# Optimization experiments

Hardware: AMD Instinct MI355X
Metric: run time of the kernel (lower is better)

## Reference

```python
import jax, jax.numpy as jnp
import numpy as np

D_MODEL = 1024
N_HEADS = 16
D_HEAD = 64
SCALE = D_HEAD ** -0.5


def setup_inputs() -> dict:
    key = jax.random.key(0)
    k1, k2, k3 = jax.random.split(key, 3)
    B, N = 4, 2048
    x = jax.random.normal(k1, (B, N, D_MODEL), dtype=jnp.float32)
    # NOTE: original torch module overwrites to_q three times, so q/k/v share ONE projection.
    W_qkv = jax.random.normal(k2, (D_MODEL, N_HEADS * D_HEAD), dtype=jnp.float32) * (D_MODEL ** -0.5)
    W_out = jax.random.normal(k3, (N_HEADS * D_HEAD, D_MODEL), dtype=jnp.float32) * (D_MODEL ** -0.5)
    b_out = jnp.zeros((D_MODEL,), dtype=jnp.float32)
    return {"x": x, "W_qkv": W_qkv, "W_out": W_out, "b_out": b_out}


def reference(x, W_qkv, W_out, b_out):
    B, N, _ = x.shape
    # shared projection (faithful to the to_q bug): q = k = v
    qkv = x @ W_qkv                                   # [B, N, H*D]
    q = qkv.reshape(B, N, N_HEADS, D_HEAD).transpose(0, 2, 1, 3)  # [B, H, N, D]
    k = q
    v = q
    scores = jnp.einsum('bhid,bhjd->bhij', q, k) * SCALE          # [B, H, N, N]
    attn = jax.nn.softmax(scores, axis=-1)
    out = jnp.einsum('bhij,bhjd->bhid', attn, v)                  # [B, H, N, D]
    out = out.transpose(0, 2, 1, 3).reshape(B, N, N_HEADS * D_HEAD)
    return out @ W_out + b_out
```

## Files before the change

### kernel.cpp

```cpp
#include <hip/hip_runtime.h>

typedef float  f32x4  __attribute__((ext_vector_type(4)));
typedef __bf16 bf16x8 __attribute__((ext_vector_type(8)));
typedef __bf16 bf16x4 __attribute__((ext_vector_type(4)));
typedef unsigned short u16x8 __attribute__((ext_vector_type(8)));

__device__ __forceinline__ unsigned short f2bf(float f) {
    unsigned u = __builtin_bit_cast(unsigned, f);
    unsigned r = u + 0x7FFFu + ((u >> 16) & 1u);
    return (unsigned short)(r >> 16);
}

__device__ __forceinline__ f32x4 mfma16(bf16x8 a, bf16x8 b, f32x4 c) {
    return __builtin_amdgcn_mfma_f32_16x16x32_bf16(a, b, c, 0, 0, 0);
}
__device__ __forceinline__ f32x4 mfma16u(u16x8 a, u16x8 b, f32x4 c) {
    return __builtin_amdgcn_mfma_f32_16x16x32_bf16(
        __builtin_bit_cast(bf16x8, a), __builtin_bit_cast(bf16x8, b), c, 0, 0, 0);
}

__device__ __forceinline__ float fexp2(float x) {
    float r;
    asm("v_exp_f32 %0, %1" : "=v"(r) : "v"(x));
    return r;
}

__device__ __forceinline__ void gload16(const void* g, void* l) {
    __builtin_amdgcn_global_load_lds((const __attribute__((address_space(1))) void*)g,
                                     (__attribute__((address_space(3))) void*)l,
                                     16, 0, 0);
}

__global__ __launch_bounds__(256) void cast_transpose2(const float* __restrict__ W0,
                                                       const float* __restrict__ W1,
                                                       __bf16* __restrict__ T0Q,
                                                       __bf16* __restrict__ T1Q) {
    const float* W = blockIdx.z ? W1 : W0;
    __bf16* Wt = blockIdx.z ? T1Q : T0Q;
    __shared__ __bf16 T[64][64];
    const int tid = threadIdx.x;
    const int k0 = blockIdx.y * 64, n0 = blockIdx.x * 64;
#pragma unroll
    for (int c = 0; c < 4; ++c) {
        int idx = c * 256 + tid;
        int kr = idx >> 4, nc = (idx & 15) * 4;
        f32x4 w = *(const f32x4*)&W[(size_t)(k0 + kr) * 1024 + n0 + nc];
        int g = ((nc >> 3) ^ (kr >> 3)) * 8 + (nc & 7);
        bf16x4 pk;
        pk[0] = (__bf16)w[0]; pk[1] = (__bf16)w[1];
        pk[2] = (__bf16)w[2]; pk[3] = (__bf16)w[3];
        *(bf16x4*)&T[kr][g] = pk;
    }
    __syncthreads();
#pragma unroll
    for (int c = 0; c < 2; ++c) {
        int idx = c * 256 + tid;
        int n = idx >> 3, k8 = (idx & 7) * 8;
        bf16x8 o;
#pragma unroll
        for (int e = 0; e < 8; ++e) {
            int k = k8 + e;
            o[e] = T[k][((n >> 3) ^ (k >> 3)) * 8 + (n & 7)];
        }
        *(bf16x8*)&Wt[(size_t)(n0 + n) * 1024 + k0 + k8] = o;
    }
}

template <bool OUT_BF16, bool WRITE_VT, bool CAST_A>
__global__ __launch_bounds__(256) void gemm_bt(const void* __restrict__ Av,
                                               const unsigned short* __restrict__ Bt,
                                               void* __restrict__ Cout,
                                               const float* __restrict__ bias,
                                               __bf16* __restrict__ vT) {
    constexpr int K = 1024, NN = 1024;
    __shared__ unsigned short SM[18432];
    typedef unsigned short u16_72[72];
    u16_72* As = (u16_72*)SM;
    u16_72* Bs = (u16_72*)(SM + 9216);
    const int tid  = threadIdx.x;
    const int lane = tid & 63, wid = tid >> 6;
    const int wm = wid >> 1, wn = wid & 1;
    const int i = lane & 15, q8 = (lane >> 4) * 8;
    const int bid = blockIdx.y * 8 + blockIdx.x;
    const int swz = (bid & 7) * 64 + (bid >> 3);
    const int tm = (swz >> 3) * 128, tn = (swz & 7) * 128;
    const int srow = tid >> 3, scol = (tid & 7) * 8;

    f32x4 acc[4][4] = {};

    for (int k0 = 0; k0 < K; k0 += 64) {
#pragma unroll
        for (int c = 0; c < 4; ++c) {
            int row = c * 32 + srow;
            u16x8 av;
            if constexpr (CAST_A) {
                const float* Af = (const float*)Av;
                const float* p = &Af[(size_t)(tm + row) * K + k0 + scol];
                f32x4 a0 = *(const f32x4*)p;
                f32x4 a1 = *(const f32x4*)(p + 4);
                av[0] = f2bf(a0[0]); av[1] = f2bf(a0[1]);
                av[2] = f2bf(a0[2]); av[3] = f2bf(a0[3]);
                av[4] = f2bf(a1[0]); av[5] = f2bf(a1[1]);
                av[6] = f2bf(a1[2]); av[7] = f2bf(a1[3]);
            } else {
                const unsigned short* Au = (const unsigned short*)Av;
                av = *(const u16x8*)&Au[(size_t)(tm + row) * K + k0 + scol];
            }
            u16x8 bv = *(const u16x8*)&Bt[(size_t)(tn + row) * K + k0 + scol];
            *(u16x8*)&As[row][scol] = av;
            *(u16x8*)&Bs[row][scol] = bv;
        }
        __syncthreads();
#pragma unroll
        for (int ks = 0; ks < 2; ++ks) {
            u16x8 af[4], bfr[4];
#pragma unroll
            for (int m = 0; m < 4; ++m) af[m]  = *(const u16x8*)&As[wm * 64 + m * 16 + i][ks * 32 + q8];
#pragma unroll
            for (int nn = 0; nn < 4; ++nn) bfr[nn] = *(const u16x8*)&Bs[wn * 64 + nn * 16 + i][ks * 32 + q8];
#pragma unroll
            for (int m = 0; m < 4; ++m)
#pragma unroll
                for (int nn = 0; nn < 4; ++nn)
                    acc[m][nn] = mfma16u(af[m], bfr[nn], acc[m][nn]);
        }
        __syncthreads();
    }

    const int r0 = (lane >> 4) * 4;
#pragma unroll
    for (int nn = 0; nn < 4; ++nn) {
        int col = tn + wn * 64 + nn * 16 + i;
        float bv = 0.f;
        if constexpr (!OUT_BF16) bv = bias[col];
#pragma unroll
        for (int m = 0; m < 4; ++m) {
            int rowb = tm + wm * 64 + m * 16 + r0;
#pragma unroll
            for (int r = 0; r < 4; ++r) {
                if constexpr (OUT_BF16)
                    ((unsigned short*)Cout)[(size_t)(rowb + r) * NN + col] = f2bf(acc[m][nn][r]);
                else
                    ((float*)Cout)[(size_t)(rowb + r) * NN + col] = acc[m][nn][r] + bv;
            }
        }
    }

    if constexpr (WRITE_VT) {
        unsigned short* T = SM;
#pragma unroll
        for (int nn = 0; nn < 4; ++nn) {
            const int col = wn * 64 + nn * 16 + i;
            const int g = col >> 3, c7 = col & 7;
#pragma unroll
            for (int m = 0; m < 4; ++m) {
                const int rbase = wm * 64 + m * 16 + r0;
                const int rsw = (rbase >> 3) & 15;
#pragma unroll
                for (int r = 0; r < 4; ++r)
                    T[(rbase + r) * 128 + ((g ^ rsw) * 8) + c7] = f2bf(acc[m][nn][r]);
            }
        }
        __syncthreads();
        const size_t vb0 = ((size_t)(tm >> 11) * 16 + (tn >> 6)) * 131072 + (size_t)(tm & 2047);
#pragma unroll
        for (int c = 0; c < 8; ++c) {
            int idx = c * 256 + tid;
            int hh = idx >> 10, dd = (idx >> 4) & 63, n8 = (idx & 15) * 8;
            int g = (hh * 64 + dd) >> 3, c7 = dd & 7, rsw = idx & 15;
            u16x8 o;
#pragma unroll
            for (int e = 0; e < 8; ++e)
                o[e] = T[(n8 + e) * 128 + ((g ^ rsw) * 8) + c7];
            *(u16x8*)&vT[vb0 + (size_t)hh * 131072 + (size_t)dd * 2048 + n8] = o;
        }
    }
}

__global__ __launch_bounds__(256, 4) void flash_attn7(const __bf16* __restrict__ qkv,
                                                      const __bf16* __restrict__ vT,
                                                      __bf16* __restrict__ attnout) {
    __shared__ __bf16 Ks[2][4096];
    __shared__ __bf16 Vs[2][4096];

    const int tid = threadIdx.x, lane = tid & 63, wid = tid >> 6;
    const int i = lane & 15, qg = lane >> 4;

    const int n = blockIdx.x;
    const int j = n & 7, t = n >> 3;
    const int head = j * 8 + (t >> 4);
    const int b = head >> 4, h = head & 15;
    const int q0 = (t & 15) * 128;

    const size_t base  = (size_t)b * (2048 * 1024) + (size_t)h * 64;
    const size_t vbase = (size_t)head * (64 * 2048);

    bf16x8 qf[2][2];
#pragma unroll
    for (int g = 0; g < 2; ++g) {
        int qrow = q0 + wid * 32 + g * 16 + i;
#pragma unroll
        for (int s = 0; s < 2; ++s)
            qf[g][s] = *(const bf16x8*)&qkv[base + (size_t)qrow * 1024 + s * 32 + qg * 8];
    }

    const int r0s = tid >> 3, g0s = tid & 7;
    const __bf16* ksrc0 = &qkv[base + (size_t)r0s * 1024 + (size_t)((g0s ^ (r0s & 7)) * 8)];
    const __bf16* ksrc1 = ksrc0 + 32 * 1024;
    const __bf16* vsrc0 = &vT[vbase + (size_t)r0s * 2048 + (size_t)((g0s ^ (r0s & 7)) * 8)];
    const __bf16* vsrc1 = vsrc0 + 32 * 2048;

    auto STAGE = [&](int buf) {
        gload16(ksrc0, &Ks[buf][wid * 512]);
        gload16(ksrc1, &Ks[buf][2048 + wid * 512]);
        gload16(vsrc0, &Vs[buf][wid * 512]);
        gload16(vsrc1, &Vs[buf][2048 + wid * 512]);
        ksrc0 += 64 * 1024; ksrc1 += 64 * 1024;
        vsrc0 += 64;        vsrc1 += 64;
    };

    const float SL2E = 0.18033688f;
    f32x4 po[2][4] = {};
    f32x4 po5[2]   = {};
    bf16x8 ones;
#pragma unroll
    for (int e = 0; e < 8; ++e) ones[e] = (__bf16)1.0f;

    auto BODY = [&](const __bf16* Kb, const __bf16* Vb) {
        __builtin_amdgcn_s_setprio(1);
        f32x4 st[2][4];
#pragma unroll
        for (int m = 0; m < 4; ++m) {
            bf16x8 kf0 = *(const bf16x8*)&Kb[(m * 16 + i) * 64 + ((qg) ^ (i & 7)) * 8];
            bf16x8 kf1 = *(const bf16x8*)&Kb[(m * 16 + i) * 64 + ((4 + qg) ^ (i & 7)) * 8];
            f32x4 z0 = {}, z1 = {};
            z0 = mfma16(kf0, qf[0][0], z0);
            st[0][m] = mfma16(kf1, qf[0][1], z0);
            z1 = mfma16(kf0, qf[1][0], z1);
            st[1][m] = mfma16(kf1, qf[1][1], z1);
        }
        __builtin_amdgcn_s_setprio(0);

        bf16x8 pa[2][2];
#pragma unroll
        for (int g = 0; g < 2; ++g) {
#pragma unroll
            for (int m = 0; m < 4; ++m)
#pragma unroll
                for (int r = 0; r < 4; ++r)
                    st[g][m][r] = fexp2(st[g][m][r] * SL2E);

#pragma unroll
            for (int r = 0; r < 4; ++r) {
                pa[g][0][r]     = (__bf16)st[g][0][r];
                pa[g][0][4 + r] = (__bf16)st[g][1][r];
                pa[g][1][r]     = (__bf16)st[g][2][r];
                pa[g][1][4 + r] = (__bf16)st[g][3][r];
            }
        }

        __builtin_amdgcn_s_setprio(1);
#pragma unroll
        for (int s = 0; s < 2; ++s) {
#pragma unroll
            for (int nf = 0; nf < 4; ++nf) {
                const int row = nf * 16 + i;
                bf16x8 vf;
                *(bf16x4*)&vf = *(const bf16x4*)
                    &Vb[row * 64 + (((s * 4 + (qg >> 1)) ^ (i & 7)) * 8 + (qg & 1) * 4)];
                *((bf16x4*)&vf + 1) = *(const bf16x4*)
                    &Vb[row * 64 + (((s * 4 + 2 + (qg >> 1)) ^ (i & 7)) * 8 + (qg & 1) * 4)];
                po[0][nf] = mfma16(pa[0][s], vf, po[0][nf]);
                po[1][nf] = mfma16(pa[1][s], vf, po[1][nf]);
            }
            po5[0] = mfma16(pa[0][s], ones, po5[0]);
            po5[1] = mfma16(pa[1][s], ones, po5[1]);
        }
        __builtin_amdgcn_s_setprio(0);
    };

    STAGE(0);
    __syncthreads();
    for (int kt2 = 0; kt2 < 16; ++kt2) {
        STAGE(1);
        BODY(Ks[0], Vs[0]);
        __syncthreads();
        if (kt2 < 15) STAGE(0);
        BODY(Ks[1], Vs[1]);
        __syncthreads();
    }

#pragma unroll
    for (int g = 0; g < 2; ++g) {
        float linv[4];
#pragma unroll
        for (int r = 0; r < 4; ++r) linv[r] = __builtin_amdgcn_rcpf(po5[g][r]);
#pragma unroll
        for (int nf = 0; nf < 4; ++nf)
#pragma unroll
            for (int r = 0; r < 4; ++r) {
                int row = q0 + wid * 32 + g * 16 + qg * 4 + r;
                attnout[base + (size_t)row * 1024 + nf * 16 + i] = (__bf16)(po[g][nf][r] * linv[r]);
            }
    }
}

extern "C" void kernel_launch(void* const* d_in, const int* in_sizes, int n_in,
                              void* d_out, int out_size, void* d_ws, size_t ws_size,
                              hipStream_t stream) {
    const float* x    = (const float*)d_in[0];
    const float* Wqkv = (const float*)d_in[1];
    const float* Wout = (const float*)d_in[2];
    const float* bout = (const float*)d_in[3];
    float* out = (float*)d_out;

    char* ws = (char*)d_ws;
    unsigned short* aout = (unsigned short*)(ws);
    unsigned short* qkvb = (unsigned short*)(ws + (16u << 20));
    __bf16*         vTp  = (__bf16*)(ws + (32u << 20));
    __bf16*         wqt  = (__bf16*)(ws + (48u << 20));
    __bf16*         wot  = (__bf16*)(ws + (50u << 20));

    cast_transpose2<<<dim3(16, 16, 2), 256, 0, stream>>>(Wqkv, Wout, wqt, wot);

    gemm_bt<true, true, true><<<dim3(8, 64), 256, 0, stream>>>(x, (const unsigned short*)wqt,
                                                               qkvb, nullptr, vTp);

    flash_attn7<<<1024, 256, 0, stream>>>((const __bf16*)qkvb, vTp, (__bf16*)aout);

    gemm_bt<false, false, false><<<dim3(8, 64), 256, 0, stream>>>(aout, (const unsigned short*)wot,
                                                                  out, bout, nullptr);
}
```

Before: 141.9 us.

## Use direct global-to-LDS loads with XOR swizzle in GEMM; prescale Q

The GEMM kernel now stages tiles through direct global-to-LDS buffer loads into an XOR-swizzled unpadded layout. Register round-trips and the padding are gone, though the cast path still converts A through registers. The attention kernel folds the softmax scale into Q when loading it, which removes a multiply per score element. The risk is a slight precision change from rounding the scaled Q to bf16.

New measurement: 140.7 us. No clear change (-0.9%).

```diff
diff --git a/kernel.cpp b/kernel.cpp
--- a/kernel.cpp
+++ b/kernel.cpp
@@ -73,61 +73,75 @@
                                                const float* __restrict__ bias,
                                                __bf16* __restrict__ vT) {
     constexpr int K = 1024, NN = 1024;
-    __shared__ unsigned short SM[18432];
-    typedef unsigned short u16_72[72];
-    u16_72* As = (u16_72*)SM;
-    u16_72* Bs = (u16_72*)(SM + 9216);
+    __shared__ unsigned short SM[16384];
     const int tid  = threadIdx.x;
     const int lane = tid & 63, wid = tid >> 6;
     const int wm = wid >> 1, wn = wid & 1;
-    const int i = lane & 15, q8 = (lane >> 4) * 8;
+    const int i = lane & 15, qg = lane >> 4;
     const int bid = blockIdx.y * 8 + blockIdx.x;
     const int swz = (bid & 7) * 64 + (bid >> 3);
     const int tm = (swz >> 3) * 128, tn = (swz & 7) * 128;
+
+    const int rl  = wid * 32 + (lane >> 3);
+    const int gsw = ((lane & 7) ^ (rl & 7)) * 8;
+    const unsigned short* Bsrc = &Bt[(size_t)(tn + rl) * K + gsw];
+    const unsigned short* Asrc = &((const unsigned short*)Av)[(size_t)(tm + rl) * K + gsw];
     const int srow = tid >> 3, scol = (tid & 7) * 8;
+    const float* Afsrc = &((const float*)Av)[(size_t)(tm + srow) * K + scol];
+    const int acol = ((scol >> 3) ^ (srow & 7)) * 8;
 
     f32x4 acc[4][4] = {};
 
-    for (int k0 = 0; k0 < K; k0 += 64) {
+    auto STAGE = [&]() {
 #pragma unroll
         for (int c = 0; c < 4; ++c) {
-            int row = c * 32 + srow;
-            u16x8 av;
             if constexpr (CAST_A) {
-                const float* Af = (const float*)Av;
-                const float* p = &Af[(size_t)(tm + row) * K + k0 + scol];
+                int row = c * 32 + srow;
+                const float* p = Afsrc + (size_t)c * 32 * K;
                 f32x4 a0 = *(const f32x4*)p;
                 f32x4 a1 = *(const f32x4*)(p + 4);
+                u16x8 av;
                 av[0] = f2bf(a0[0]); av[1] = f2bf(a0[1]);
                 av[2] = f2bf(a0[2]); av[3] = f2bf(a0[3]);
                 av[4] = f2bf(a1[0]); av[5] = f2bf(a1[1]);
                 av[6] = f2bf(a1[2]); av[7] = f2bf(a1[3]);
+                *(u16x8*)&SM[row * 64 + acol] = av;
             } else {
-                const unsigned short* Au = (const unsigned short*)Av;
-                av = *(const u16x8*)&Au[(size_t)(tm + row) * K + k0 + scol];
-            }
-            u16x8 bv = *(const u16x8*)&Bt[(size_t)(tn + row) * K + k0 + scol];
-            *(u16x8*)&As[row][scol] = av;
-            *(u16x8*)&Bs[row][scol] = bv;
-        }
-        __syncthreads();
+                gload16(Asrc + (size_t)c * 8 * K, &SM[(wid * 32 + c * 8) * 64]);
+            }
+            gload16(Bsrc + (size_t)c * 8 * K, &SM[8192 + (wid * 32 + c * 8) * 64]);
+        }
+        Afsrc += 64; Asrc += 64; Bsrc += 64;
+    };
+
+    auto COMP = [&]() {
+        const unsigned short* As = SM;
+        const unsigned short* Bs = SM + 8192;
 #pragma unroll
         for (int ks = 0; ks < 2; ++ks) {
             u16x8 af[4], bfr[4];
 #pragma unroll
-            for (int m = 0; m < 4; ++m) af[m]  = *(const u16x8*)&As[wm * 64 + m * 16 + i][ks * 32 + q8];
-#pragma unroll
-            for (int nn = 0; nn < 4; ++nn) bfr[nn] = *(const u16x8*)&Bs[wn * 64 + nn * 16 + i][ks * 32 + q8];
+            for (int m = 0; m < 4; ++m)
+                af[m]  = *(const u16x8*)&As[(wm * 64 + m * 16 + i) * 64 + (((ks * 4 + qg) ^ (i & 7)) * 8)];
+#pragma unroll
+            for (int nn = 0; nn < 4; ++nn)
+                bfr[nn] = *(const u16x8*)&Bs[(wn * 64 + nn * 16 + i) * 64 + (((ks * 4 + qg) ^ (i & 7)) * 8)];
 #pragma unroll
             for (int m = 0; m < 4; ++m)
 #pragma unroll
                 for (int nn = 0; nn < 4; ++nn)
                     acc[m][nn] = mfma16u(af[m], bfr[nn], acc[m][nn]);
         }
-        __syncthreads();
-    }
-
-    const int r0 = (lane >> 4) * 4;
+    };
+
+    for (int kk = 0; kk < 16; ++kk) {
+        STAGE();
+        __syncthreads();
+        COMP();
+        __syncthreads();
+    }
+
+    const int r0 = qg * 4;
 #pragma unroll
     for (int nn = 0; nn < 4; ++nn) {
         int col = tn + wn * 64 + nn * 16 + i;
@@ -177,7 +191,7 @@
     }
 }
 
-__global__ __launch_bounds__(256, 4) void flash_attn7(const __bf16* __restrict__ qkv,
+__global__ __launch_bounds__(256, 4) void flash_attn9(const __bf16* __restrict__ qkv,
                                                       const __bf16* __restrict__ vT,
                                                       __bf16* __restrict__ attnout) {
     __shared__ __bf16 Ks[2][4096];
@@ -195,13 +209,19 @@
     const size_t base  = (size_t)b * (2048 * 1024) + (size_t)h * 64;
     const size_t vbase = (size_t)head * (64 * 2048);
 
+    const float SL2E = 0.18033688f;
+
     bf16x8 qf[2][2];
 #pragma unroll
     for (int g = 0; g < 2; ++g) {
         int qrow = q0 + wid * 32 + g * 16 + i;
 #pragma unroll
-        for (int s = 0; s < 2; ++s)
-            qf[g][s] = *(const bf16x8*)&qkv[base + (size_t)qrow * 1024 + s * 32 + qg * 8];
+        for (int s = 0; s < 2; ++s) {
+            bf16x8 tq = *(const bf16x8*)&qkv[base + (size_t)qrow * 1024 + s * 32 + qg * 8];
+#pragma unroll
+            for (int e = 0; e < 8; ++e)
+                qf[g][s][e] = (__bf16)((float)tq[e] * SL2E);
+        }
     }
 
     const int r0s = tid >> 3, g0s = tid & 7;
@@ -219,7 +239,6 @@
         vsrc0 += 64;        vsrc1 += 64;
     };
 
-    const float SL2E = 0.18033688f;
     f32x4 po[2][4] = {};
     f32x4 po5[2]   = {};
     bf16x8 ones;
@@ -248,7 +267,7 @@
             for (int m = 0; m < 4; ++m)
 #pragma unroll
                 for (int r = 0; r < 4; ++r)
-                    st[g][m][r] = fexp2(st[g][m][r] * SL2E);
+                    st[g][m][r] = fexp2(st[g][m][r]);
 
 #pragma unroll
             for (int r = 0; r < 4; ++r) {
@@ -326,7 +345,7 @@
     gemm_bt<true, true, true><<<dim3(8, 64), 256, 0, stream>>>(x, (const unsigned short*)wqt,
                                                                qkvb, nullptr, vTp);
 
-    flash_attn7<<<1024, 256, 0, stream>>>((const __bf16*)qkvb, vTp, (__bf16*)aout);
+    flash_attn9<<<1024, 256, 0, stream>>>((const __bf16*)qkvb, vTp, (__bf16*)aout);
 
     gemm_bt<false, false, false><<<dim3(8, 64), 256, 0, stream>>>(aout, (const unsigned short*)wot,
                                                                   out, bout, nullptr);
```
